# Optimization experiments

Measured on AMD Instinct MI355X. Metric: run time of the kernel, lower is better.

## Reference

```python
import jax, jax.numpy as jnp
import numpy as np

T = 2048          # tokens
HIDDEN = 2048
FFN = 1024
E = 16            # routed experts
ZERO = 16         # zero experts
NTOT = E + ZERO   # router output dim
K = 4             # top-k
SCALE = 2.5       # routed_scaling_factor


def setup_inputs() -> dict:
    key = jax.random.key(0)
    k0, k1, k2, k3, k4 = jax.random.split(key, 5)
    return {
        "hidden_states": jax.random.normal(k0, (T, HIDDEN), jnp.float32),
        "router_w": jax.random.normal(k1, (NTOT, HIDDEN), jnp.float32) * 0.02,
        "e_score_correction_bias": jax.random.normal(k2, (NTOT,), jnp.float32) * 0.01,
        "w13": jax.random.normal(k3, (E, HIDDEN, 2 * FFN), jnp.float32) * 0.02,
        "w2": jax.random.normal(k4, (E, FFN, HIDDEN), jnp.float32) * 0.02,
    }


def reference(hidden_states, router_w, e_score_correction_bias, w13, w2):
    # ---- router: fp32 linear -> softmax -> bias-corrected top-k ----
    logits = hidden_states @ router_w.T                      # [T, NTOT]
    scores = jax.nn.softmax(logits, axis=-1)
    scores_for_choice = scores + e_score_correction_bias[None, :]
    topk_w, topk_ids = jax.lax.top_k(scores_for_choice, K)   # [T, K]
    topk_w = topk_w * SCALE

    # ---- zero-expert masking: ids >= E are identity experts ----
    zero_mask = topk_ids >= E
    zero_total = jnp.sum(jnp.where(zero_mask, topk_w, 0.0), axis=-1, keepdims=True)
    zero_expert_output = hidden_states * zero_total          # [T, HIDDEN]
    topk_ids = jnp.where(zero_mask, 0, topk_ids)
    topk_w = jnp.where(zero_mask, 0.0, topk_w)

    # ---- combine weights scattered to dense [T, E] (top-k ids unique per row;
    # masked duplicates at id 0 carry weight 0 so .add is exact) ----
    comb = jnp.zeros((hidden_states.shape[0], E), jnp.float32)
    comb = comb.at[jnp.arange(hidden_states.shape[0])[:, None], topk_ids].add(topk_w)

    # ---- grouped-GEMM experts expressed densely: gate_up -> swiglu -> down ----
    gate_up = jnp.einsum('th,ehf->tef', hidden_states, w13)  # [T, E, 2*FFN]
    gate, up = jnp.split(gate_up, 2, axis=-1)
    act = jax.nn.silu(gate) * up                             # npu_swiglu
    expert_out = jnp.einsum('tef,efh->teh', act, w2)         # [T, E, HIDDEN]

    routed = jnp.einsum('te,teh->th', comb, expert_out)
    return routed + zero_expert_output
```

## Files before the change

### kernel.cpp

```cpp
#include <hip/hip_runtime.h>
#include <hip/hip_bf16.h>
#include <math.h>

#define TOKENS 2048
#define HID 2048
#define FFN 1024
#define NEXP 16
#define NTOT 32
#define KSEL 4
#define RSCALE 2.5f

typedef __bf16 v8bf __attribute__((ext_vector_type(8)));
typedef float v4f __attribute__((ext_vector_type(4)));
typedef unsigned short u16x8v __attribute__((ext_vector_type(8)));

static __device__ __forceinline__ v8bf zero_v8bf() {
  u16x8v z = {0, 0, 0, 0, 0, 0, 0, 0};
  return __builtin_bit_cast(v8bf, z);
}

static __device__ __forceinline__ int swz(int row, int chunk) {
  return (row << 6) + ((((unsigned)(chunk ^ row)) & 7u) << 3);
}

__global__ __launch_bounds__(256) void router_kernel(
    const float* __restrict__ hidden, const float* __restrict__ rw,
    const float* __restrict__ bias, float* __restrict__ out,
    __bf16* __restrict__ hbf,
    int* __restrict__ counts, int* __restrict__ pair_token,
    float* __restrict__ pair_weight)
{
  const int t = blockIdx.x;
  const int tid = threadIdx.x;
  __shared__ float sh[HID];
  __shared__ float part[8][NTOT];
  __shared__ float s_zt;

  const float* hrow = hidden + (size_t)t * HID;
  for (int i = tid; i < HID / 4; i += 256)
    ((float4*)sh)[i] = ((const float4*)hrow)[i];
  __syncthreads();

  {
    const int base = tid * 8;
    v8bf v;
#pragma unroll
    for (int j = 0; j < 8; ++j) v[j] = (__bf16)sh[base + j];
    *(v8bf*)(hbf + (size_t)t * HID + base) = v;
  }

  {
    const int g = tid >> 5, e = tid & 31;
    const float* w = rw + (size_t)e * HID + g * 256;
    const float* hh = sh + g * 256;
    float acc = 0.f;
#pragma unroll 8
    for (int h = 0; h < 256; ++h) acc = fmaf(hh[h], w[h], acc);
    part[g][e] = acc;
  }
  __syncthreads();

  if (tid < 64) {
    const int lane = tid;
    float logit = -INFINITY;
    if (lane < NTOT) {
      float s = 0.f;
#pragma unroll
      for (int g = 0; g < 8; ++g) s += part[g][lane];
      logit = s;
    }
    float m = logit;
#pragma unroll
    for (int off = 32; off; off >>= 1) m = fmaxf(m, __shfl_xor(m, off));
    const float ex = (lane < NTOT) ? expf(logit - m) : 0.f;
    float sum = ex;
#pragma unroll
    for (int off = 32; off; off >>= 1) sum += __shfl_xor(sum, off);
    float sc = (lane < NTOT) ? (ex / sum + bias[lane]) : -INFINITY;

    float zt = 0.f;
#pragma unroll
    for (int it = 0; it < KSEL; ++it) {
      float v = sc; int vid = lane;
#pragma unroll
      for (int off = 32; off; off >>= 1) {
        const float ov = __shfl_xor(v, off);
        const int oid = __shfl_xor(vid, off);
        if (ov > v || (ov == v && oid < vid)) { v = ov; vid = oid; }
      }
      const float wv = v * RSCALE;
      if (vid >= NEXP) {
        zt += wv;
      } else if (lane == 0) {
        const int pos = atomicAdd(&counts[vid], 1);
        pair_token[vid * TOKENS + pos] = t;
        pair_weight[vid * TOKENS + pos] = wv;
      }
      if (lane == vid) sc = -INFINITY;
    }
    if (lane == 0) s_zt = zt;
  }
  __syncthreads();

  const float zt = s_zt;
  float* orow = out + (size_t)t * HID;
  for (int i = tid; i < HID / 4; i += 256) {
    float4 v = ((const float4*)sh)[i];
    v.x *= zt; v.y *= zt; v.z *= zt; v.w *= zt;
    ((float4*)orow)[i] = v;
  }
}

__global__ void scan_kernel(const int* __restrict__ counts,
                            int* __restrict__ offsets) {
  if (threadIdx.x == 0) {
    int acc = 0;
#pragma unroll
    for (int e = 0; e < NEXP; ++e) { offsets[e] = acc; acc += counts[e]; }
    offsets[NEXP] = acc;
  }
}

__global__ __launch_bounds__(256, 4) void gemm1_kernel(
    const __bf16* __restrict__ hbf, const float* __restrict__ w13,
    const int* __restrict__ counts, const int* __restrict__ offsets,
    const int* __restrict__ pair_token, const float* __restrict__ pair_weight,
    __bf16* __restrict__ act)
{
  const int lin = blockIdx.x;
  const int xcd = lin & 7;
  const int q = lin >> 3;
  const int mt = q & 31;
  const int g = (q >> 5) * 8 + xcd;
  const int ft = g & 15;
  const int e = g >> 4;

  const int cnt = counts[e];
  const int m0 = mt * 64;
  if (m0 >= cnt) return;
  const int obase = offsets[e];
  const int fbase = ft * 64;

  __shared__ __bf16 sA[64 * 64];
  __shared__ __bf16 sB[128 * 64];
  __shared__ int sTok[64];
  __shared__ float sW[64];

  const int tid = threadIdx.x;
  if (tid < 64) {
    const int m = m0 + tid;
    sTok[tid] = (m < cnt) ? pair_token[e * TOKENS + m] : -1;
    sW[tid] = (m < cnt) ? pair_weight[e * TOKENS + m] : 0.f;
  }
  __syncthreads();

  const int wid = tid >> 6, lane = tid & 63;
  const int wr = wid >> 1, wf = wid & 1;
  const int lrow = lane & 15, lq = lane >> 4;

  const int ar = tid >> 2, ac = (tid & 3) * 2;
  const int a_tok = sTok[ar];
  const __bf16* a_src =
      (a_tok >= 0) ? (hbf + (size_t)a_tok * HID + ac * 8) : nullptr;

  const int h = lane >> 5;
  const int f_off = (wid >> 1) * 32 + (lane & 31);
  const int brow = h * 64 + f_off;
  const int bc0 = (wid & 1) * 4;
  const float* b_ptr = w13 + (size_t)e * HID * (2 * FFN)
                     + (size_t)((wid & 1) * 32) * (2 * FFN)
                     + h * FFN + fbase + f_off;

  v4f accg[2][2], accu[2][2];
#pragma unroll
  for (int mi = 0; mi < 2; ++mi)
#pragma unroll
    for (int fi = 0; fi < 2; ++fi) {
      v4f z = {0.f, 0.f, 0.f, 0.f};
      accg[mi][fi] = z; accu[mi][fi] = z;
    }

  for (int kt = 0; kt < HID; kt += 64) {
    if (a_tok >= 0) {
      const v8bf* s = (const v8bf*)(a_src + kt);
      *(v8bf*)&sA[swz(ar, ac)] = s[0];
      *(v8bf*)&sA[swz(ar, ac + 1)] = s[1];
    } else {
      *(v8bf*)&sA[swz(ar, ac)] = zero_v8bf();
      *(v8bf*)&sA[swz(ar, ac + 1)] = zero_v8bf();
    }
    {
      const float* src = b_ptr + (size_t)kt * (2 * FFN);
      float pb[32];
#pragma unroll
      for (int j = 0; j < 32; ++j) pb[j] = src[(size_t)j * (2 * FFN)];
#pragma unroll
      for (int c = 0; c < 4; ++c) {
        v8bf v;
#pragma unroll
        for (int j = 0; j < 8; ++j) v[j] = (__bf16)pb[c * 8 + j];
        *(v8bf*)&sB[swz(brow, bc0 + c)] = v;
      }
    }
    __syncthreads();

#pragma unroll
    for (int ks = 0; ks < 2; ++ks) {
      v8bf a[2], bg[2], bu[2];
#pragma unroll
      for (int mi = 0; mi < 2; ++mi)
        a[mi] = *(const v8bf*)&sA[swz(wr * 32 + mi * 16 + lrow, ks * 4 + lq)];
#pragma unroll
      for (int fi = 0; fi < 2; ++fi) {
        bg[fi] = *(const v8bf*)&sB[swz(wf * 32 + fi * 16 + lrow, ks * 4 + lq)];
        bu[fi] = *(const v8bf*)&sB[swz(64 + wf * 32 + fi * 16 + lrow, ks * 4 + lq)];
      }
#pragma unroll
      for (int mi = 0; mi < 2; ++mi)
#pragma unroll
        for (int fi = 0; fi < 2; ++fi) {
          accg[mi][fi] = __builtin_amdgcn_mfma_f32_16x16x32_bf16(
              a[mi], bg[fi], accg[mi][fi], 0, 0, 0);
          accu[mi][fi] = __builtin_amdgcn_mfma_f32_16x16x32_bf16(
              a[mi], bu[fi], accu[mi][fi], 0, 0, 0);
        }
    }
    __syncthreads();
  }

#pragma unroll
  for (int mi = 0; mi < 2; ++mi) {
#pragma unroll
    for (int fi = 0; fi < 2; ++fi) {
      const int f = fbase + wf * 32 + fi * 16 + lrow;
#pragma unroll
      for (int r = 0; r < 4; ++r) {
        const int lr = wr * 32 + mi * 16 + lq * 4 + r;
        const int m = m0 + lr;
        if (m < cnt) {
          const float gg = accg[mi][fi][r];
          const float uu = accu[mi][fi][r];
          const float sg = gg / (1.f + __expf(-gg));
          act[(size_t)(obase + m) * FFN + f] = (__bf16)(sg * uu * sW[lr]);
        }
      }
    }
  }
}

__global__ __launch_bounds__(256, 4) void gemm2_kernel(
    const __bf16* __restrict__ act, const float* __restrict__ w2,
    const int* __restrict__ counts, const int* __restrict__ offsets,
    const int* __restrict__ pair_token, float* __restrict__ out)
{
  const int lin = blockIdx.x;
  const int xcd = lin & 7;
  const int q = lin >> 3;
  const int mt = q & 31;
  const int g = (q >> 5) * 8 + xcd;
  const int nt = g & 31;
  const int e = g >> 5;

  const int cnt = counts[e];
  const int m0 = mt * 64;
  if (m0 >= cnt) return;
  const int obase = offsets[e];
  const int n0 = nt * 64;

  __shared__ __bf16 sA[64 * 64];
  __shared__ __bf16 sB[64 * 64];
  __shared__ int sTok[64];

  const int tid = threadIdx.x;
  if (tid < 64) {
    const int m = m0 + tid;
    sTok[tid] = (m < cnt) ? pair_token[e * TOKENS + m] : -1;
  }
  __syncthreads();

  const int wid = tid >> 6, lane = tid & 63;
  const int wr = wid >> 1, wf = wid & 1;
  const int lrow = lane & 15, lq = lane >> 4;

  const int ar = tid >> 2, ac = (tid & 3) * 2;
  const bool avalid = (m0 + ar) < cnt;
  const __bf16* a_src =
      avalid ? (act + (size_t)(obase + m0 + ar) * FFN + ac * 8) : nullptr;

  const int n_off = (wid >> 1) * 32 + (lane & 31);
  const int bk0 = (wid & 1) * 32 + (lane >> 5) * 16;
  const int bc0 = bk0 >> 3;
  const float* b_ptr = w2 + (size_t)e * FFN * HID
                     + (size_t)bk0 * HID + n0 + n_off;

  v4f acc[2][2];
#pragma unroll
  for (int mi = 0; mi < 2; ++mi)
#pragma unroll
    for (int ni = 0; ni < 2; ++ni) {
      v4f z = {0.f, 0.f, 0.f, 0.f};
      acc[mi][ni] = z;
    }

  for (int kt = 0; kt < FFN; kt += 64) {
    if (avalid) {
      const v8bf* s = (const v8bf*)(a_src + kt);
      *(v8bf*)&sA[swz(ar, ac)] = s[0];
      *(v8bf*)&sA[swz(ar, ac + 1)] = s[1];
    } else {
      *(v8bf*)&sA[swz(ar, ac)] = zero_v8bf();
      *(v8bf*)&sA[swz(ar, ac + 1)] = zero_v8bf();
    }
    {
      const float* src = b_ptr + (size_t)kt * HID;
      float pb[16];
#pragma unroll
      for (int j = 0; j < 16; ++j) pb[j] = src[(size_t)j * HID];
#pragma unroll
      for (int c = 0; c < 2; ++c) {
        v8bf v;
#pragma unroll
        for (int j = 0; j < 8; ++j) v[j] = (__bf16)pb[c * 8 + j];
        *(v8bf*)&sB[swz(n_off, bc0 + c)] = v;
      }
    }
    __syncthreads();

#pragma unroll
    for (int ks = 0; ks < 2; ++ks) {
      v8bf a[2], b[2];
#pragma unroll
      for (int mi = 0; mi < 2; ++mi)
        a[mi] = *(const v8bf*)&sA[swz(wr * 32 + mi * 16 + lrow, ks * 4 + lq)];
#pragma unroll
      for (int ni = 0; ni < 2; ++ni)
        b[ni] = *(const v8bf*)&sB[swz(wf * 32 + ni * 16 + lrow, ks * 4 + lq)];
#pragma unroll
      for (int mi = 0; mi < 2; ++mi)
#pragma unroll
        for (int ni = 0; ni < 2; ++ni)
          acc[mi][ni] = __builtin_amdgcn_mfma_f32_16x16x32_bf16(
              a[mi], b[ni], acc[mi][ni], 0, 0, 0);
    }
    __syncthreads();
  }

#pragma unroll
  for (int mi = 0; mi < 2; ++mi) {
#pragma unroll
    for (int ni = 0; ni < 2; ++ni) {
      const int n = n0 + wf * 32 + ni * 16 + lrow;
#pragma unroll
      for (int r = 0; r < 4; ++r) {
        const int lr = wr * 32 + mi * 16 + lq * 4 + r;
        const int m = m0 + lr;
        if (m < cnt) {
          const int t = sTok[lr];
          atomicAdd(&out[(size_t)t * HID + n], acc[mi][ni][r]);
        }
      }
    }
  }
}

extern "C" void kernel_launch(void* const* d_in, const int* in_sizes, int n_in,
                              void* d_out, int out_size, void* d_ws, size_t ws_size,
                              hipStream_t stream) {
  const float* hidden = (const float*)d_in[0];
  const float* rw     = (const float*)d_in[1];
  const float* bias   = (const float*)d_in[2];
  const float* w13    = (const float*)d_in[3];
  const float* w2     = (const float*)d_in[4];
  float* out = (float*)d_out;

  char* ws = (char*)d_ws;
  int* counts = (int*)ws;
  int* offsets = (int*)(ws + 64);
  int* pair_token = (int*)(ws + 256);
  float* pair_weight = (float*)(ws + 256 + (size_t)NEXP * TOKENS * 4);
  __bf16* hbf = (__bf16*)(ws + 256 + 2 * (size_t)NEXP * TOKENS * 4);
  __bf16* act = hbf + (size_t)TOKENS * HID;

  hipMemsetAsync(counts, 0, 16 * sizeof(int), stream);
  router_kernel<<<TOKENS, 256, 0, stream>>>(hidden, rw, bias, out, hbf,
                                            counts, pair_token, pair_weight);
  scan_kernel<<<1, 64, 0, stream>>>(counts, offsets);
  gemm1_kernel<<<8192, 256, 0, stream>>>(
      hbf, w13, counts, offsets, pair_token, pair_weight, act);
  gemm2_kernel<<<16384, 256, 0, stream>>>(
      act, w2, counts, offsets, pair_token, out);
}
```

Baseline: 347.4 us.

## Vectorize fp32 weight loads, remap blocks per expert to XCD, enlarge gemm2 M tile

Both expert GEMMs now load the fp32 weight tiles as float4 vectors along the contiguous N dimension and transpose them in registers before writing bf16 to shared memory. Previously each thread issued strided scalar loads. The block-index decode now pins each expert to one XCD, so that expert's weights stay in a single L2. gemm2 also doubles its M tile to 128 rows, which halves the grid and the number of times the w2 tile is reloaded. The cost is more registers per thread and narrower shared-memory stores in gemm2.

```diff
diff --git a/kernel.cpp b/kernel.cpp
--- a/kernel.cpp
+++ b/kernel.cpp
@@ -11,6 +11,7 @@
 #define RSCALE 2.5f
 
 typedef __bf16 v8bf __attribute__((ext_vector_type(8)));
+typedef __bf16 v4bf __attribute__((ext_vector_type(4)));
 typedef float v4f __attribute__((ext_vector_type(4)));
 typedef unsigned short u16x8v __attribute__((ext_vector_type(8)));
 
@@ -130,10 +131,11 @@
   const int lin = blockIdx.x;
   const int xcd = lin & 7;
   const int q = lin >> 3;
-  const int mt = q & 31;
-  const int g = (q >> 5) * 8 + xcd;
-  const int ft = g & 15;
-  const int e = g >> 4;
+  const int d = q & 511;
+  const int ehi = q >> 9;
+  const int mt = d & 31;
+  const int ft = d >> 5;
+  const int e = ehi * 8 + xcd;
 
   const int cnt = counts[e];
   const int m0 = mt * 64;
@@ -163,13 +165,11 @@
   const __bf16* a_src =
       (a_tok >= 0) ? (hbf + (size_t)a_tok * HID + ac * 8) : nullptr;
 
-  const int h = lane >> 5;
-  const int f_off = (wid >> 1) * 32 + (lane & 31);
-  const int brow = h * 64 + f_off;
-  const int bc0 = (wid & 1) * 4;
+  const int rg = tid & 31, kg = tid >> 5;
+  const int brow0 = rg * 4;
+  const int fb = (rg < 16) ? (fbase + rg * 4) : (FFN + fbase + (rg - 16) * 4);
   const float* b_ptr = w13 + (size_t)e * HID * (2 * FFN)
-                     + (size_t)((wid & 1) * 32) * (2 * FFN)
-                     + h * FFN + fbase + f_off;
+                     + (size_t)(kg * 8) * (2 * FFN) + fb;
 
   v4f accg[2][2], accu[2][2];
 #pragma unroll
@@ -181,26 +181,28 @@
     }
 
   for (int kt = 0; kt < HID; kt += 64) {
+    float pb[8][4];
+    {
+      const float* src = b_ptr + (size_t)kt * (2 * FFN);
+#pragma unroll
+      for (int j = 0; j < 8; ++j)
+        *(float4*)pb[j] = *(const float4*)(src + (size_t)j * (2 * FFN));
+    }
+    v8bf pa0, pa1;
     if (a_tok >= 0) {
       const v8bf* s = (const v8bf*)(a_src + kt);
-      *(v8bf*)&sA[swz(ar, ac)] = s[0];
-      *(v8bf*)&sA[swz(ar, ac + 1)] = s[1];
+      pa0 = s[0]; pa1 = s[1];
     } else {
-      *(v8bf*)&sA[swz(ar, ac)] = zero_v8bf();
-      *(v8bf*)&sA[swz(ar, ac + 1)] = zero_v8bf();
-    }
-    {
-      const float* src = b_ptr + (size_t)kt * (2 * FFN);
-      float pb[32];
-#pragma unroll
-      for (int j = 0; j < 32; ++j) pb[j] = src[(size_t)j * (2 * FFN)];
-#pragma unroll
-      for (int c = 0; c < 4; ++c) {
-        v8bf v;
-#pragma unroll
-        for (int j = 0; j < 8; ++j) v[j] = (__bf16)pb[c * 8 + j];
-        *(v8bf*)&sB[swz(brow, bc0 + c)] = v;
-      }
+      pa0 = zero_v8bf(); pa1 = zero_v8bf();
+    }
+    *(v8bf*)&sA[swz(ar, ac)] = pa0;
+    *(v8bf*)&sA[swz(ar, ac + 1)] = pa1;
+#pragma unroll
+    for (int i = 0; i < 4; ++i) {
+      v8bf v;
+#pragma unroll
+      for (int j = 0; j < 8; ++j) v[j] = (__bf16)pb[j][i];
+      *(v8bf*)&sB[swz(brow0 + i, kg)] = v;
     }
     __syncthreads();
 
@@ -256,23 +258,24 @@
   const int lin = blockIdx.x;
   const int xcd = lin & 7;
   const int q = lin >> 3;
-  const int mt = q & 31;
-  const int g = (q >> 5) * 8 + xcd;
-  const int nt = g & 31;
-  const int e = g >> 5;
+  const int d = q & 511;
+  const int ehi = q >> 9;
+  const int mt = d & 15;
+  const int nt = d >> 4;
+  const int e = ehi * 8 + xcd;
 
   const int cnt = counts[e];
-  const int m0 = mt * 64;
+  const int m0 = mt * 128;
   if (m0 >= cnt) return;
   const int obase = offsets[e];
   const int n0 = nt * 64;
 
-  __shared__ __bf16 sA[64 * 64];
+  __shared__ __bf16 sA[128 * 64];
   __shared__ __bf16 sB[64 * 64];
-  __shared__ int sTok[64];
+  __shared__ int sTok[128];
 
   const int tid = threadIdx.x;
-  if (tid < 64) {
+  if (tid < 128) {
     const int m = m0 + tid;
     sTok[tid] = (m < cnt) ? pair_token[e * TOKENS + m] : -1;
   }
@@ -282,20 +285,19 @@
   const int wr = wid >> 1, wf = wid & 1;
   const int lrow = lane & 15, lq = lane >> 4;
 
-  const int ar = tid >> 2, ac = (tid & 3) * 2;
+  const int ar = tid >> 1, ac4 = (tid & 1) * 4;
   const bool avalid = (m0 + ar) < cnt;
   const __bf16* a_src =
-      avalid ? (act + (size_t)(obase + m0 + ar) * FFN + ac * 8) : nullptr;
-
-  const int n_off = (wid >> 1) * 32 + (lane & 31);
-  const int bk0 = (wid & 1) * 32 + (lane >> 5) * 16;
-  const int bc0 = bk0 >> 3;
+      avalid ? (act + (size_t)(obase + m0 + ar) * FFN + ac4 * 8) : nullptr;
+
+  const int rg = tid & 15, kg = tid >> 4;
+  const int brow0 = rg * 4;
   const float* b_ptr = w2 + (size_t)e * FFN * HID
-                     + (size_t)bk0 * HID + n0 + n_off;
-
-  v4f acc[2][2];
-#pragma unroll
-  for (int mi = 0; mi < 2; ++mi)
+                     + (size_t)(kg * 4) * HID + n0 + rg * 4;
+
+  v4f acc[4][2];
+#pragma unroll
+  for (int mi = 0; mi < 4; ++mi)
 #pragma unroll
     for (int ni = 0; ni < 2; ++ni) {
       v4f z = {0.f, 0.f, 0.f, 0.f};
@@ -303,40 +305,44 @@
     }
 
   for (int kt = 0; kt < FFN; kt += 64) {
+    float pb[4][4];
+    {
+      const float* src = b_ptr + (size_t)kt * HID;
+#pragma unroll
+      for (int j = 0; j < 4; ++j)
+        *(float4*)pb[j] = *(const float4*)(src + (size_t)j * HID);
+    }
+    v8bf pa[4];
     if (avalid) {
       const v8bf* s = (const v8bf*)(a_src + kt);
-      *(v8bf*)&sA[swz(ar, ac)] = s[0];
-      *(v8bf*)&sA[swz(ar, ac + 1)] = s[1];
+#pragma unroll
+      for (int c = 0; c < 4; ++c) pa[c] = s[c];
     } else {
-      *(v8bf*)&sA[swz(ar, ac)] = zero_v8bf();
-      *(v8bf*)&sA[swz(ar, ac + 1)] = zero_v8bf();
-    }
-    {
-      const float* src = b_ptr + (size_t)kt * HID;
-      float pb[16];
-#pragma unroll
-      for (int j = 0; j < 16; ++j) pb[j] = src[(size_t)j * HID];
-#pragma unroll
-      for (int c = 0; c < 2; ++c) {
-        v8bf v;
-#pragma unroll
-        for (int j = 0; j < 8; ++j) v[j] = (__bf16)pb[c * 8 + j];
-        *(v8bf*)&sB[swz(n_off, bc0 + c)] = v;
-      }
+#pragma unroll
+      for (int c = 0; c < 4; ++c) pa[c] = zero_v8bf();
+    }
+#pragma unroll
+    for (int c = 0; c < 4; ++c) *(v8bf*)&sA[swz(ar, ac4 + c)] = pa[c];
+#pragma unroll
+    for (int i = 0; i < 4; ++i) {
+      v4bf v;
+#pragma unroll
+      for (int j = 0; j < 4; ++j) v[j] = (__bf16)pb[j][i];
+      *(v4bf*)&sB[swz(brow0 + i, kg >> 1) + (kg & 1) * 4] = v;
     }
     __syncthreads();
 
 #pragma unroll
     for (int ks = 0; ks < 2; ++ks) {
-      v8bf a[2], b[2];
-#pragma unroll
-      for (int mi = 0; mi < 2; ++mi)
-        a[mi] = *(const v8bf*)&sA[swz(wr * 32 + mi * 16 + lrow, ks * 4 + lq)];
+      v8bf a[4], b[2];
+#pragma unroll
+      for (int mi = 0; mi < 4; ++mi)
+        a[mi] = *(const v8bf*)&sA[swz(wr * 64 + mi * 16 + lrow, ks * 4 + lq)];
 #pragma unroll
       for (int ni = 0; ni < 2; ++ni)
         b[ni] = *(const v8bf*)&sB[swz(wf * 32 + ni * 16 + lrow, ks * 4 + lq)];
 #pragma unroll
-      for (int mi = 0; mi < 2; ++mi)
+      for (int mi = 0; mi < 4; ++mi)
 #pragma unroll
         for (int ni = 0; ni < 2; ++ni)
           acc[mi][ni] = __builtin_amdgcn_mfma_f32_16x16x32_bf16(
@@ -346,13 +352,13 @@
   }
 
 #pragma unroll
-  for (int mi = 0; mi < 2; ++mi) {
+  for (int mi = 0; mi < 4; ++mi) {
 #pragma unroll
     for (int ni = 0; ni < 2; ++ni) {
       const int n = n0 + wf * 32 + ni * 16 + lrow;
 #pragma unroll
       for (int r = 0; r < 4; ++r) {
-        const int lr = wr * 32 + mi * 16 + lq * 4 + r;
+        const int lr = wr * 64 + mi * 16 + lq * 4 + r;
         const int m = m0 + lr;
         if (m < cnt) {
           const int t = sTok[lr];
@@ -387,6 +393,6 @@
   scan_kernel<<<1, 64, 0, stream>>>(counts, offsets);
   gemm1_kernel<<<8192, 256, 0, stream>>>(
       hbf, w13, counts, offsets, pair_token, pair_weight, act);
-  gemm2_kernel<<<16384, 256, 0, stream>>>(
+  gemm2_kernel<<<8192, 256, 0, stream>>>(
       act, w2, counts, offsets, pair_token, out);
 }
```

After: 353.1 us. Within noise of the previous version (+1.7%).
